# Optimization experiments

Hardware: AMD Instinct MI355X
Metric: run time of the kernel (lower is better)

The kernel has to match this reference:

```python
import jax, jax.numpy as jnp
import numpy as np

HEAD_DIM = 72
NUM_HEADS = 16
EPS = 1e-6
ROPE_THETA = 10000.0


def _rms_norm(x, scale):
    # normalize over last dim in fp32, apply learned scale
    xf = x.astype(jnp.float32)
    normed = xf * jax.lax.rsqrt(jnp.mean(xf * xf, axis=-1, keepdims=True) + EPS)
    return (normed * scale.astype(jnp.float32)).astype(x.dtype)


def _rope_cos_sin(pixel_position_ids, dtype):
    # pixel_position_ids: [B, N, 2] -> cos/sin [B, N, head_dim]
    dim = HEAD_DIM // 2                      # 36
    inv_freq = 1.0 / (ROPE_THETA ** (jnp.arange(0, dim, 2, dtype=jnp.float32) / dim))  # [18]
    pos = pixel_position_ids.astype(jnp.float32)          # [B, N, 2]
    freqs = pos[..., None] * inv_freq                      # [B, N, 2, 18]
    emb = jnp.concatenate([freqs, freqs], axis=-1)         # [B, N, 2, 36]
    cos = jnp.cos(emb)
    sin = jnp.sin(emb)
    # concat x-axis and y-axis halves -> [B, N, 72]
    cos = cos.reshape(cos.shape[0], cos.shape[1], -1)
    sin = sin.reshape(sin.shape[0], sin.shape[1], -1)
    return cos.astype(dtype), sin.astype(dtype)


def _rotate_half(x):
    half = x.shape[-1] // 2
    return jnp.concatenate([-x[..., half:], x[..., :half]], axis=-1)


def _apply_2d_rope(x, cos, sin):
    # x: [B, N, H, Dh]; cos/sin: [B, N, Dh] split into 2 spatial halves of 36 channels each
    cpd = 2 * (x.shape[-1] // 4)             # channels_per_dim = 36
    outs = []
    for k in range(2):
        xk = x[..., k * cpd:(k + 1) * cpd]
        ck = cos[:, :, None, k * cpd:(k + 1) * cpd]   # broadcast over heads (unsqueeze_dim=2)
        sk = sin[:, :, None, k * cpd:(k + 1) * cpd]
        outs.append(xk * ck + _rotate_half(xk) * sk)
    return jnp.concatenate(outs, axis=-1)


def reference(hidden_states, pixel_position_ids, Wq, Wk, Wv, Wo, q_scale, k_scale, v_scale):
    B, N, D = hidden_states.shape
    H, Dh = NUM_HEADS, HEAD_DIM
    scaling = Dh ** -0.5

    q = (hidden_states @ Wq).reshape(B, N, H, Dh)
    k = (hidden_states @ Wk).reshape(B, N, H, Dh)
    v = (hidden_states @ Wv).reshape(B, N, H, Dh)

    q = _rms_norm(q, q_scale)
    k = _rms_norm(k, k_scale)
    v = _rms_norm(v, v_scale)

    cos, sin = _rope_cos_sin(pixel_position_ids, hidden_states.dtype)
    q = _apply_2d_rope(q, cos, sin)
    k = _apply_2d_rope(k, cos, sin)

    # full softmax attention: [B, H, N, N]
    attn = jnp.einsum('bnhd,bmhd->bhnm', q, k) * scaling
    attn = jax.nn.softmax(attn, axis=-1)
    out = jnp.einsum('bhnm,bmhd->bnhd', attn, v).reshape(B, N, H * Dh)
    return out @ Wo


def setup_inputs() -> dict:
    key = jax.random.key(0)
    k1, k2, k3, k4, k5, k6 = jax.random.split(key, 6)
    B, N, D = 8, 1024, 1152
    grid = 32  # 448 / 14
    return {
        'hidden_states': jax.random.normal(k1, (B, N, D), dtype=jnp.float32),
        'pixel_position_ids': jax.random.randint(k2, (B, N, 2), 0, grid, dtype=jnp.int32),
        'Wq': jax.random.normal(k3, (D, D), dtype=jnp.float32) * 0.02,
        'Wk': jax.random.normal(k4, (D, D), dtype=jnp.float32) * 0.02,
        'Wv': jax.random.normal(k5, (D, D), dtype=jnp.float32) * 0.02,
        'Wo': jax.random.normal(k6, (D, D), dtype=jnp.float32) * 0.02,
        'q_scale': jnp.ones((HEAD_DIM,), dtype=jnp.float32),
        'k_scale': jnp.ones((HEAD_DIM,), dtype=jnp.float32),
        'v_scale': jnp.ones((HEAD_DIM,), dtype=jnp.float32),
    }
```

## Files before the change

### kernel.cpp

```cpp
#include <hip/hip_runtime.h>
#include <hip/hip_bf16.h>

typedef unsigned short u16;
typedef __attribute__((ext_vector_type(8))) short bf16x8;
typedef __attribute__((ext_vector_type(8))) unsigned short u16x8;
typedef __attribute__((ext_vector_type(4))) float f32x4;

#define NTOK 8192
#define DMODEL 1152
#define NHEAD 16
#define DHEAD 72
#define DPAD 96
#define VROWS 80
#define NQKV 3456

__device__ __forceinline__ u16 f2bf(float f){
  __hip_bfloat16 h = __float2bfloat16(f);
  return *reinterpret_cast<u16*>(&h);
}
__device__ __forceinline__ float bf2f(u16 u){
  union { unsigned int i; float f; } v; v.i = ((unsigned int)u) << 16; return v.f;
}
__device__ __forceinline__ void gload16(const void* g, void* l){
  __builtin_amdgcn_global_load_lds((const __attribute__((address_space(1))) void*)g,
                                   (__attribute__((address_space(3))) void*)l, 16, 0, 0);
}

__global__ __launch_bounds__(256) void cvt_x(const float* __restrict__ X, u16* __restrict__ Xb){
  int i = (blockIdx.x * 256 + threadIdx.x) * 8;
  float4 a = *(const float4*)(X + i);
  float4 b = *(const float4*)(X + i + 4);
  u16x8 o;
  o[0]=f2bf(a.x); o[1]=f2bf(a.y); o[2]=f2bf(a.z); o[3]=f2bf(a.w);
  o[4]=f2bf(b.x); o[5]=f2bf(b.y); o[6]=f2bf(b.z); o[7]=f2bf(b.w);
  *(u16x8*)(Xb + i) = o;
}

__global__ __launch_bounds__(256) void pack_w(const float* __restrict__ Wq, const float* __restrict__ Wk,
                                              const float* __restrict__ Wv, const float* __restrict__ Wo,
                                              u16* __restrict__ WT){
  __shared__ u16 t[32][33];
  int tx = threadIdx.x & 31, ty = threadIdx.x >> 5;
  int k0 = blockIdx.x * 32, n0 = blockIdx.y * 32;
  int ng = n0 + tx;
  const float* W; int nl;
  if (ng < 1152)      { W = Wq; nl = ng; }
  else if (ng < 2304) { W = Wk; nl = ng - 1152; }
  else if (ng < 3456) { W = Wv; nl = ng - 2304; }
  else                { W = Wo; nl = ng - 3456; }
  #pragma unroll
  for (int i = 0; i < 4; i++)
    t[ty + i*8][tx] = f2bf(W[(size_t)(k0 + ty + i*8) * 1152 + nl]);
  __syncthreads();
  #pragma unroll
  for (int i = 0; i < 4; i++)
    WT[(size_t)(n0 + ty + i*8) * 1152 + k0 + tx] = t[tx][ty + i*8];
}

__global__ __launch_bounds__(256) void rope_tab(const int* __restrict__ pid,
                                                float* __restrict__ tc, float* __restrict__ ts){
  int i = blockIdx.x * 256 + threadIdx.x;
  if (i >= NTOK * 36) return;
  int tok = i / 36, r = i - tok * 36;
  int c = r / 18, j = r - c * 18;
  float freq = exp2f(-0.7382062433f * (float)j);
  float ang = (float)pid[tok * 2 + c] * freq;
  float s, co;
  sincosf(ang, &s, &co);
  tc[i] = co; ts[i] = s;
}

template<int FP32OUT>
__global__ __launch_bounds__(256) void gemm_bt(const u16* __restrict__ A, const u16* __restrict__ Bt,
                                               void* __restrict__ C, int Ncols){
  __shared__ u16 Al[128 * 64];
  __shared__ u16 Bl[128 * 64];
  int tid = threadIdx.x, lane = tid & 63, w = tid >> 6;
  int wr = w >> 1, wc = w & 1, l16 = lane & 15, lq = lane >> 4;
  int m0 = blockIdx.x * 128, n0 = blockIdx.y * 128;
  f32x4 acc[4][4] = {};
  int grow = lane >> 3;
  int gchunk = (lane & 7) ^ grow;
  const char* Abase = (const char*)A  + (size_t)(m0 + grow) * 2304 + gchunk * 16;
  const char* Bbase = (const char*)Bt + (size_t)(n0 + grow) * 2304 + gchunk * 16;
  int sw = l16 & 7;
  for (int kt = 0; kt < 18; ++kt){
    __syncthreads();
    #pragma unroll
    for (int i = 0; i < 4; i++){
      int j = w * 4 + i;
      gload16(Abase + (size_t)j * 8 * 2304 + kt * 128, &Al[j * 512]);
      gload16(Bbase + (size_t)j * 8 * 2304 + kt * 128, &Bl[j * 512]);
    }
    __syncthreads();
    #pragma unroll
    for (int kk = 0; kk < 2; kk++){
      bf16x8 af[4], bfr[4];
      #pragma unroll
      for (int m = 0; m < 4; m++){
        int row = wr * 64 + m * 16 + l16;
        af[m] = *(const bf16x8*)&Al[row * 64 + (((kk * 4 + lq) ^ sw) * 8)];
      }
      #pragma unroll
      for (int n = 0; n < 4; n++){
        int row = wc * 64 + n * 16 + l16;
        bfr[n] = *(const bf16x8*)&Bl[row * 64 + (((kk * 4 + lq) ^ sw) * 8)];
      }
      #pragma unroll
      for (int m = 0; m < 4; m++)
        #pragma unroll
        for (int n = 0; n < 4; n++)
          acc[m][n] = __builtin_amdgcn_mfma_f32_16x16x32_bf16(af[m], bfr[n], acc[m][n], 0, 0, 0);
    }
  }
  #pragma unroll
  for (int m = 0; m < 4; m++)
    #pragma unroll
    for (int n = 0; n < 4; n++)
      #pragma unroll
      for (int r = 0; r < 4; r++){
        int row = m0 + wr * 64 + m * 16 + lq * 4 + r;
        int col = n0 + wc * 64 + n * 16 + l16;
        if (FP32OUT) ((float*)C)[(size_t)row * Ncols + col] = acc[m][n][r];
        else         ((u16*)  C)[(size_t)row * Ncols + col] = f2bf(acc[m][n][r]);
      }
}

__global__ __launch_bounds__(256) void rmsrope(const u16* __restrict__ QKV,
    const float* __restrict__ tc, const float* __restrict__ ts,
    const float* __restrict__ qsc, const float* __restrict__ ksc, const float* __restrict__ vsc,
    u16* __restrict__ Qp, u16* __restrict__ Kp, u16* __restrict__ Vt){
  __shared__ u16 vl[72][264];
  int h = blockIdx.y, tid = threadIdx.x;
  int tok = blockIdx.x * 256 + tid;
  int b = tok >> 10, n = tok & 1023;
  int n0 = (blockIdx.x & 3) * 256;
  int bh = b * NHEAD + h;
  const u16* base = QKV + (size_t)tok * NQKV + h * DHEAD;

  {
    u16x8 vr[9];
    #pragma unroll
    for (int i = 0; i < 9; i++) vr[i] = *(const u16x8*)(base + 2304 + i * 8);
    float ss = 0.f;
    #pragma unroll
    for (int i = 0; i < 9; i++)
      #pragma unroll
      for (int e = 0; e < 8; e++){ float f = bf2f(vr[i][e]); ss += f * f; }
    float rv = rsqrtf(ss * (1.f / 72.f) + 1e-6f);
    #pragma unroll
    for (int i = 0; i < 9; i++)
      #pragma unroll
      for (int e = 0; e < 8; e++){
        int d = i * 8 + e;
        vl[d][tid] = f2bf(bf2f(vr[i][e]) * rv * vsc[d]);
      }
  }
  #pragma unroll
  for (int qk = 0; qk < 2; ++qk){
    const u16* src = base + qk * 1152;
    const float* sc = qk ? ksc : qsc;
    u16* dst = qk ? Kp : Qp;
    u16x8 xr[9];
    #pragma unroll
    for (int i = 0; i < 9; i++) xr[i] = *(const u16x8*)(src + i * 8);
    float ss = 0.f;
    #pragma unroll
    for (int i = 0; i < 9; i++)
      #pragma unroll
      for (int e = 0; e < 8; e++){ float f = bf2f(xr[i][e]); ss += f * f; }
    float rs_ = rsqrtf(ss * (1.f / 72.f) + 1e-6f);
    float x[72];
    #pragma unroll
    for (int i = 0; i < 9; i++)
      #pragma unroll
      for (int e = 0; e < 8; e++){ int d = i * 8 + e; x[d] = bf2f(xr[i][e]) * rs_ * sc[d]; }
    #pragma unroll
    for (int c = 0; c < 2; c++)
      #pragma unroll
      for (int j = 0; j < 18; j++){
        float co = tc[(size_t)tok * 36 + c * 18 + j];
        float si = ts[(size_t)tok * 36 + c * 18 + j];
        float x1 = x[c * 36 + j], x2 = x[c * 36 + j + 18];
        x[c * 36 + j]      = x1 * co - x2 * si;
        x[c * 36 + j + 18] = x2 * co + x1 * si;
      }
    size_t off = ((size_t)bh * 1024 + n) * DPAD;
    #pragma unroll
    for (int i = 0; i < 9; i++){
      u16x8 o;
      #pragma unroll
      for (int e = 0; e < 8; e++) o[e] = f2bf(x[i * 8 + e]);
      *(u16x8*)(dst + off + i * 8) = o;
    }
    u16x8 z = {0,0,0,0,0,0,0,0};
    #pragma unroll
    for (int i = 9; i < 12; i++) *(u16x8*)(dst + off + i * 8) = z;
  }
  __syncthreads();
  u16x8 z = {0,0,0,0,0,0,0,0};
  for (int c = tid; c < VROWS * 32; c += 256){
    int row = c >> 5, seg = c & 31;
    u16x8 v = z;
    if (row < 72) v = *(const u16x8*)&vl[row][seg * 8];
    *(u16x8*)(Vt + ((size_t)bh * VROWS + row) * 1024 + n0 + seg * 8) = v;
  }
}

__global__ __launch_bounds__(512) void attn(const u16* __restrict__ Qp, const u16* __restrict__ Kp,
                                            const u16* __restrict__ Vt, u16* __restrict__ AO){
  __shared__ u16 Kl[64][104];
  __shared__ u16 Vl[VROWS][72];
  __shared__ u16 Pl[8][16][72];
  int tid = threadIdx.x, lane = tid & 63, w = tid >> 6;
  int l16 = lane & 15, lq = lane >> 4;
  int bh = blockIdx.y, b = bh >> 4, h = bh & 15;
  int q0 = blockIdx.x * 128;
  const u16* Qb = Qp + (size_t)bh * 1024 * DPAD;
  const u16* Kb = Kp + (size_t)bh * 1024 * DPAD;
  const u16* Vb = Vt + (size_t)bh * VROWS * 1024;

  int qrow = q0 + w * 16 + l16;
  bf16x8 qf[3];
  #pragma unroll
  for (int ks = 0; ks < 3; ks++)
    qf[ks] = *(const bf16x8*)(Qb + (size_t)qrow * DPAD + ks * 32 + lq * 8);

  f32x4 accO[5] = {};
  float mrow[4] = {-1e30f, -1e30f, -1e30f, -1e30f};
  float lrow[4] = {0.f, 0.f, 0.f, 0.f};
  const float scl = 0.1178511302f;

  for (int kv = 0; kv < 16; ++kv){
    __syncthreads();
    for (int c = tid; c < 768; c += 512){
      int row = c / 12, col = c - row * 12;
      *(u16x8*)&Kl[row][col * 8] = *(const u16x8*)(Kb + (size_t)(kv * 64 + row) * DPAD + col * 8);
    }
    for (int c = tid; c < VROWS * 8; c += 512){
      int row = c >> 3, seg = c & 7;
      *(u16x8*)&Vl[row][seg * 8] = *(const u16x8*)(Vb + (size_t)row * 1024 + kv * 64 + seg * 8);
    }
    __syncthreads();

    f32x4 accS[4] = {};
    #pragma unroll
    for (int j = 0; j < 4; j++)
      #pragma unroll
      for (int ks = 0; ks < 3; ks++){
        bf16x8 kf = *(const bf16x8*)&Kl[j * 16 + l16][ks * 32 + lq * 8];
        accS[j] = __builtin_amdgcn_mfma_f32_16x16x32_bf16(qf[ks], kf, accS[j], 0, 0, 0);
      }
    float alpha[4], rsum[4];
    #pragma unroll
    for (int r = 0; r < 4; r++){
      float v = fmaxf(fmaxf(accS[0][r], accS[1][r]), fmaxf(accS[2][r], accS[3][r]));
      v = fmaxf(v, __shfl_xor(v, 1)); v = fmaxf(v, __shfl_xor(v, 2));
      v = fmaxf(v, __shfl_xor(v, 4)); v = fmaxf(v, __shfl_xor(v, 8));
      float mn = fmaxf(mrow[r], v * scl);
      alpha[r] = __expf(mrow[r] - mn);
      mrow[r] = mn;
      rsum[r] = 0.f;
    }
    #pragma unroll
    for (int j = 0; j < 4; j++)
      #pragma unroll
      for (int r = 0; r < 4; r++){
        float p = __expf(accS[j][r] * scl - mrow[r]);
        rsum[r] += p;
        Pl[w][lq * 4 + r][j * 16 + l16] = f2bf(p);
      }
    #pragma unroll
    for (int r = 0; r < 4; r++){
      float s = rsum[r];
      s += __shfl_xor(s, 1); s += __shfl_xor(s, 2);
      s += __shfl_xor(s, 4); s += __shfl_xor(s, 8);
      lrow[r] = lrow[r] * alpha[r] + s;
    }
    #pragma unroll
    for (int nf = 0; nf < 5; nf++)
      #pragma unroll
      for (int r = 0; r < 4; r++) accO[nf][r] *= alpha[r];
    #pragma unroll
    for (int ks = 0; ks < 2; ks++){
      bf16x8 pf = *(const bf16x8*)&Pl[w][l16][ks * 32 + lq * 8];
      #pragma unroll
      for (int nf = 0; nf < 5; nf++){
        bf16x8 vf = *(const bf16x8*)&Vl[nf * 16 + l16][ks * 32 + lq * 8];
        accO[nf] = __builtin_amdgcn_mfma_f32_16x16x32_bf16(pf, vf, accO[nf], 0, 0, 0);
      }
    }
  }
  #pragma unroll
  for (int r = 0; r < 4; r++){
    float inv = 1.f / lrow[r];
    int qg = q0 + w * 16 + lq * 4 + r;
    size_t rowoff = ((size_t)(b * 1024 + qg)) * DMODEL + h * DHEAD;
    #pragma unroll
    for (int nf = 0; nf < 5; nf++){
      int d = nf * 16 + l16;
      if (d < 72) AO[rowoff + d] = f2bf(accO[nf][r] * inv);
    }
  }
}

extern "C" void kernel_launch(void* const* d_in, const int* in_sizes, int n_in,
                              void* d_out, int out_size, void* d_ws, size_t ws_size,
                              hipStream_t stream){
  const float* X   = (const float*)d_in[0];
  const int*   pid = (const int*)  d_in[1];
  const float* Wq  = (const float*)d_in[2];
  const float* Wk  = (const float*)d_in[3];
  const float* Wv  = (const float*)d_in[4];
  const float* Wo  = (const float*)d_in[5];
  const float* qsc = (const float*)d_in[6];
  const float* ksc = (const float*)d_in[7];
  const float* vsc = (const float*)d_in[8];
  char* ws = (char*)d_ws;
  u16*   Xb  = (u16*)(ws);
  u16*   WT  = (u16*)(ws + 18874368);
  u16*   QKV = (u16*)(ws + 29491200);
  u16*   Qp  = (u16*)(ws + 86114304);
  u16*   Kp  = (u16*)(ws + 111280128);
  u16*   Vt  = (u16*)(ws + 136445952);
  float* tc  = (float*)(ws + 157417472);
  float* tsn = (float*)(ws + 158597120);
  u16*   AO  = QKV;

  cvt_x  <<<4608, 256, 0, stream>>>(X, Xb);
  pack_w <<<dim3(36, 144), 256, 0, stream>>>(Wq, Wk, Wv, Wo, WT);
  rope_tab<<<1152, 256, 0, stream>>>(pid, tc, tsn);
  gemm_bt<0><<<dim3(64, 27), 256, 0, stream>>>(Xb, WT, QKV, 3456);
  rmsrope<<<dim3(32, 16), 256, 0, stream>>>(QKV, tc, tsn, qsc, ksc, vsc, Qp, Kp, Vt);
  attn   <<<dim3(8, 128), 512, 0, stream>>>(Qp, Kp, Vt, AO);
  gemm_bt<1><<<dim3(64, 9), 256, 0, stream>>>(AO, WT + (size_t)3456 * 1152, d_out, 1152);
}
```

Baseline: 435.3 us.

## Drop online-softmax max tracking, fold scale into Q, sum via ones row in V

The softmax scale and log2(e) are folded into Q during the RMS-norm/RoPE pass, so the attention kernel can use exp2 directly with no running max, rescaling or shuffle reductions. Row sums come from an extra row of ones placed in the padded V tile, so the PV MFMA produces the denominator for free. Each wave now handles two 16-row query tiles, which doubles K/V reuse per shared-memory load and halves the number of blocks. Skipping max subtraction is safe only because RMS-normed Q and K keep the logits bounded; large q/k scale values could overflow exp.

```diff
diff --git a/kernel.cpp b/kernel.cpp
--- a/kernel.cpp
+++ b/kernel.cpp
@@ -161,6 +161,7 @@
     const u16* src = base + qk * 1152;
     const float* sc = qk ? ksc : qsc;
     u16* dst = qk ? Kp : Qp;
+    float fold = qk ? 1.0f : 0.17002219f;
     u16x8 xr[9];
     #pragma unroll
     for (int i = 0; i < 9; i++) xr[i] = *(const u16x8*)(src + i * 8);
@@ -190,7 +191,7 @@
     for (int i = 0; i < 9; i++){
       u16x8 o;
       #pragma unroll
-      for (int e = 0; e < 8; e++) o[e] = f2bf(x[i * 8 + e]);
+      for (int e = 0; e < 8; e++) o[e] = f2bf(x[i * 8 + e] * fold);
       *(u16x8*)(dst + off + i * 8) = o;
     }
     u16x8 z = {0,0,0,0,0,0,0,0};
@@ -199,37 +200,38 @@
   }
   __syncthreads();
   u16x8 z = {0,0,0,0,0,0,0,0};
+  u16x8 on = {0x3F80,0x3F80,0x3F80,0x3F80,0x3F80,0x3F80,0x3F80,0x3F80};
   for (int c = tid; c < VROWS * 32; c += 256){
     int row = c >> 5, seg = c & 31;
-    u16x8 v = z;
-    if (row < 72) v = *(const u16x8*)&vl[row][seg * 8];
+    u16x8 v;
+    if (row < 72)       v = *(const u16x8*)&vl[row][seg * 8];
+    else if (row == 72) v = on;
+    else                v = z;
     *(u16x8*)(Vt + ((size_t)bh * VROWS + row) * 1024 + n0 + seg * 8) = v;
   }
 }
 
-__global__ __launch_bounds__(512) void attn(const u16* __restrict__ Qp, const u16* __restrict__ Kp,
-                                            const u16* __restrict__ Vt, u16* __restrict__ AO){
+__global__ __launch_bounds__(512, 4) void attn(const u16* __restrict__ Qp, const u16* __restrict__ Kp,
+                                               const u16* __restrict__ Vt, u16* __restrict__ AO){
   __shared__ u16 Kl[64][104];
   __shared__ u16 Vl[VROWS][72];
-  __shared__ u16 Pl[8][16][72];
+  __shared__ u16 Pl[8][32][72];
   int tid = threadIdx.x, lane = tid & 63, w = tid >> 6;
   int l16 = lane & 15, lq = lane >> 4;
   int bh = blockIdx.y, b = bh >> 4, h = bh & 15;
-  int q0 = blockIdx.x * 128;
+  int q0 = blockIdx.x * 256;
   const u16* Qb = Qp + (size_t)bh * 1024 * DPAD;
   const u16* Kb = Kp + (size_t)bh * 1024 * DPAD;
   const u16* Vb = Vt + (size_t)bh * VROWS * 1024;
 
-  int qrow = q0 + w * 16 + l16;
-  bf16x8 qf[3];
-  #pragma unroll
-  for (int ks = 0; ks < 3; ks++)
-    qf[ks] = *(const bf16x8*)(Qb + (size_t)qrow * DPAD + ks * 32 + lq * 8);
-
-  f32x4 accO[5] = {};
-  float mrow[4] = {-1e30f, -1e30f, -1e30f, -1e30f};
-  float lrow[4] = {0.f, 0.f, 0.f, 0.f};
-  const float scl = 0.1178511302f;
+  bf16x8 qf[2][3];
+  #pragma unroll
+  for (int mt = 0; mt < 2; mt++)
+    #pragma unroll
+    for (int ks = 0; ks < 3; ks++)
+      qf[mt][ks] = *(const bf16x8*)(Qb + (size_t)(q0 + w * 32 + mt * 16 + l16) * DPAD + ks * 32 + lq * 8);
+
+  f32x4 accO[2][5] = {};
 
   for (int kv = 0; kv < 16; ++kv){
     __syncthreads();
@@ -243,65 +245,48 @@
     }
     __syncthreads();
 
-    f32x4 accS[4] = {};
+    f32x4 accS[2][4] = {};
     #pragma unroll
     for (int j = 0; j < 4; j++)
       #pragma unroll
       for (int ks = 0; ks < 3; ks++){
         bf16x8 kf = *(const bf16x8*)&Kl[j * 16 + l16][ks * 32 + lq * 8];
-        accS[j] = __builtin_amdgcn_mfma_f32_16x16x32_bf16(qf[ks], kf, accS[j], 0, 0, 0);
-      }
-    float alpha[4], rsum[4];
-    #pragma unroll
-    for (int r = 0; r < 4; r++){
-      float v = fmaxf(fmaxf(accS[0][r], accS[1][r]), fmaxf(accS[2][r], accS[3][r]));
-      v = fmaxf(v, __shfl_xor(v, 1)); v = fmaxf(v, __shfl_xor(v, 2));
-      v = fmaxf(v, __shfl_xor(v, 4)); v = fmaxf(v, __shfl_xor(v, 8));
-      float mn = fmaxf(mrow[r], v * scl);
-      alpha[r] = __expf(mrow[r] - mn);
-      mrow[r] = mn;
-      rsum[r] = 0.f;
-    }
-    #pragma unroll
-    for (int j = 0; j < 4; j++)
-      #pragma unroll
-      for (int r = 0; r < 4; r++){
-        float p = __expf(accS[j][r] * scl - mrow[r]);
-        rsum[r] += p;
-        Pl[w][lq * 4 + r][j * 16 + l16] = f2bf(p);
-      }
-    #pragma unroll
-    for (int r = 0; r < 4; r++){
-      float s = rsum[r];
-      s += __shfl_xor(s, 1); s += __shfl_xor(s, 2);
-      s += __shfl_xor(s, 4); s += __shfl_xor(s, 8);
-      lrow[r] = lrow[r] * alpha[r] + s;
-    }
-    #pragma unroll
-    for (int nf = 0; nf < 5; nf++)
-      #pragma unroll
-      for (int r = 0; r < 4; r++) accO[nf][r] *= alpha[r];
+        accS[0][j] = __builtin_amdgcn_mfma_f32_16x16x32_bf16(qf[0][ks], kf, accS[0][j], 0, 0, 0);
+        accS[1][j] = __builtin_amdgcn_mfma_f32_16x16x32_bf16(qf[1][ks], kf, accS[1][j], 0, 0, 0);
+      }
+    #pragma unroll
+    for (int mt = 0; mt < 2; mt++)
+      #pragma unroll
+      for (int j = 0; j < 4; j++)
+        #pragma unroll
+        for (int r = 0; r < 4; r++)
+          Pl[w][mt * 16 + lq * 4 + r][j * 16 + l16] = f2bf(exp2f(accS[mt][j][r]));
     #pragma unroll
     for (int ks = 0; ks < 2; ks++){
-      bf16x8 pf = *(const bf16x8*)&Pl[w][l16][ks * 32 + lq * 8];
+      bf16x8 pf0 = *(const bf16x8*)&Pl[w][l16][ks * 32 + lq * 8];
+      bf16x8 pf1 = *(const bf16x8*)&Pl[w][16 + l16][ks * 32 + lq * 8];
       #pragma unroll
       for (int nf = 0; nf < 5; nf++){
         bf16x8 vf = *(const bf16x8*)&Vl[nf * 16 + l16][ks * 32 + lq * 8];
-        accO[nf] = __builtin_amdgcn_mfma_f32_16x16x32_bf16(pf, vf, accO[nf], 0, 0, 0);
-      }
-    }
-  }
-  #pragma unroll
-  for (int r = 0; r < 4; r++){
-    float inv = 1.f / lrow[r];
-    int qg = q0 + w * 16 + lq * 4 + r;
-    size_t rowoff = ((size_t)(b * 1024 + qg)) * DMODEL + h * DHEAD;
-    #pragma unroll
-    for (int nf = 0; nf < 5; nf++){
-      int d = nf * 16 + l16;
-      if (d < 72) AO[rowoff + d] = f2bf(accO[nf][r] * inv);
-    }
-  }
+        accO[0][nf] = __builtin_amdgcn_mfma_f32_16x16x32_bf16(pf0, vf, accO[0][nf], 0, 0, 0);
+        accO[1][nf] = __builtin_amdgcn_mfma_f32_16x16x32_bf16(pf1, vf, accO[1][nf], 0, 0, 0);
+      }
+    }
+  }
+  #pragma unroll
+  for (int mt = 0; mt < 2; mt++)
+    #pragma unroll
+    for (int r = 0; r < 4; r++){
+      float s = __shfl(accO[mt][4][r], (lane & 48) + 8);
+      float inv = 1.f / s;
+      int qg = q0 + w * 32 + mt * 16 + lq * 4 + r;
+      size_t rowoff = ((size_t)(b * 1024 + qg)) * DMODEL + h * DHEAD;
+      #pragma unroll
+      for (int nf = 0; nf < 5; nf++){
+        int d = nf * 16 + l16;
+        if (d < 72) AO[rowoff + d] = f2bf(accO[mt][nf][r] * inv);
+      }
+    }
 }
 
 extern "C" void kernel_launch(void* const* d_in, const int* in_sizes, int n_in,
@@ -332,6 +317,6 @@
   rope_tab<<<1152, 256, 0, stream>>>(pid, tc, tsn);
   gemm_bt<0><<<dim3(64, 27), 256, 0, stream>>>(Xb, WT, QKV, 3456);
   rmsrope<<<dim3(32, 16), 256, 0, stream>>>(QKV, tc, tsn, qsc, ksc, vsc, Qp, Kp, Vt);
-  attn   <<<dim3(8, 128), 512, 0, stream>>>(Qp, Kp, Vt, AO);
+  attn   <<<dim3(4, 128), 512, 0, stream>>>(Qp, Kp, Vt, AO);
   gemm_bt<1><<<dim3(64, 9), 256, 0, stream>>>(AO, WT + (size_t)3456 * 1152, d_out, 1152);
 }
```

Measured after the change: 375.0 us. 13.9% less time.
